# Optimization experiments

Hardware: AMD Instinct MI355X
Metric: run time of the kernel (lower is better)

Reference implementation:

```python
import jax, jax.numpy as jnp
import numpy as np

NM = 16  # n_modes


def setup_inputs() -> dict:
    key = jax.random.key(0)
    k1, k2, k3, k4 = jax.random.split(key, 4)
    B, M, N, I, O = 8, 256, 256, 64, 64
    std = 1.0 / (I * O)
    x = jax.random.normal(k1, (B, M, N, I), dtype=jnp.float32)
    w1 = jax.random.normal(k2, (I, O, NM, NM, 2), dtype=jnp.float32) * std
    w2 = jax.random.normal(k3, (I, O, NM, NM, 2), dtype=jnp.float32) * std
    lin_w = jax.random.normal(k4, (O, O), dtype=jnp.float32) * (1.0 / np.sqrt(O))
    lin_b = jnp.zeros((O,), dtype=jnp.float32)
    return {"x": x, "w1": w1, "w2": w2, "lin_w": lin_w, "lin_b": lin_b}


def _to_complex(w):
    return jax.lax.complex(w[..., 0], w[..., 1])


def reference(x, w1, w2, lin_w, lin_b):
    B, M, N, I = x.shape
    O = w1.shape[1]
    # [B, I, M, N]
    xt = jnp.transpose(x, (0, 3, 1, 2))
    # rfft over last two dims -> [B, I, M, N//2 + 1] complex
    x_ft = jnp.fft.rfft2(xt, s=(M, N), axes=(-2, -1))
    w1c = _to_complex(w1)  # [I, O, NM, NM]
    w2c = _to_complex(w2)
    # truncated complex matmuls over low modes (top rows) and high-negative modes (bottom rows)
    out_top = jnp.einsum('bixy,ioxy->boxy', x_ft[:, :, :NM, :NM], w1c)
    out_bot = jnp.einsum('bixy,ioxy->boxy', x_ft[:, :, -NM:, :NM], w2c)
    zeros_mid = jnp.zeros((B, O, M - 2 * NM, NM), dtype=out_top.dtype)
    rows = jnp.concatenate([out_top, zeros_mid, out_bot], axis=2)  # [B, O, M, NM]
    zeros_right = jnp.zeros((B, O, M, N // 2 + 1 - NM), dtype=out_top.dtype)
    out_ft = jnp.concatenate([rows, zeros_right], axis=3)  # [B, O, M, N//2+1]
    y = jnp.fft.irfft2(out_ft, s=(M, N), axes=(-2, -1))  # real [B, O, M, N]
    y = jnp.transpose(y, (0, 2, 3, 1))  # [B, M, N, O]
    res = y @ lin_w + lin_b
    return jax.nn.relu(y + res)
```

## Files before the change

### kernel.cpp

```cpp
#include <hip/hip_runtime.h>
#include <hip/hip_bf16.h>
#include <math.h>


#define TOFF  65536
#define XOFF  (TOFF + 4194304)
#define YOFF  (XOFF + 524288)
#define GOFF  (YOFF + 524288)

__global__ __launch_bounds__(256) void setup_tables(const float* __restrict__ lin_w,
                                                    float* __restrict__ ws) {
    int j = blockIdx.x * 256 + threadIdx.x;
    const float ANG = 0.024543692606170259f;
    if (j < 4096) {
        int n = j >> 4, ky = j & 15;
        int a = (n * ky) & 255;
        float s, c; sincosf(ANG * (float)a, &s, &c);
        int w = ky >> 2, jj = ky & 3;
        float* p = ws + w * 2048 + n * 8 + jj * 2;
        p[0] = c; p[1] = -s;
    } else if (j < 12288) {
        int e = j - 4096; int m = e >> 5, kx = e & 31;
        int kxe = kx + (kx < 16 ? 0 : 224);
        int a = (m * kxe) & 255;
        float s, c; sincosf(ANG * (float)a, &s, &c);
        int g = kx >> 2, kl = kx & 3;
        float* p = ws + 8192 + g * 2048 + m * 8 + kl * 2;
        p[0] = c; p[1] = -s;
    } else if (j < 20480) {
        int e = j - 12288; int kx = e >> 8, m = e & 255;
        int kxe = kx + (kx < 16 ? 0 : 224);
        int a = (kxe * m) & 255;
        float s, c; sincosf(ANG * (float)a, &s, &c);
        float* p = ws + 24576 + (kx * 256 + m) * 2;
        p[0] = c * (1.0f / 256.0f);
        p[1] = s * (1.0f / 256.0f);
    } else if (j < 28672) {
        int e = j - 20480; int f = e >> 8, n = e & 255;
        int ky = f >> 1, h = f & 1;
        int a = (ky * n) & 255;
        float s, c; sincosf(ANG * (float)a, &s, &c);
        float scale = (ky == 0 ? 1.0f : 2.0f) * (1.0f / 256.0f);
        ws[40960 + f * 256 + n] = h ? (-scale * s) : (scale * c);
    } else if (j < 32768) {
        int e = j - 28672;
        int op = e >> 6, o = e & 63;
        ws[49152 + e] = lin_w[e] + ((op == o) ? 1.0f : 0.0f);
    }
}

__global__ __launch_bounds__(256) void stageA(const float* __restrict__ x,
                                              const float* __restrict__ tabA,
                                              float* __restrict__ T) {
    __shared__ float xs[8192];
    int bid = blockIdx.x;
    int b = bid >> 8, m = bid & 255;
    int t = threadIdx.x;
    int i = t & 63, w = t >> 6;
    int lane = i;
    const float* twp = tabA + __builtin_amdgcn_readfirstlane(w * 2048);
    float aR[4], aI[4];
#pragma unroll
    for (int j = 0; j < 4; ++j) { aR[j] = 0.f; aI[j] = 0.f; }
    const float* xbase = x + (size_t)bid * 16384;
#pragma unroll
    for (int c = 0; c < 2; ++c) {
        if (c) __syncthreads();
        {
            const float* gsrc = xbase + c * 8192 + (w * 8) * 256 + lane * 4;
            float* ldst = xs + (w * 8) * 256;
#pragma unroll
            for (int q = 0; q < 8; ++q) {
                __builtin_amdgcn_global_load_lds(
                    (const __attribute__((address_space(1))) void*)(gsrc + q * 256),
                    (__attribute__((address_space(3))) void*)(uintptr_t)(ldst + q * 256),
                    16, 0, 0);
            }
        }
        asm volatile("s_waitcnt vmcnt(0)" ::: "memory");
        __syncthreads();
        const float* tc = twp + c * 1024;
#pragma unroll 4
        for (int nn = 0; nn < 128; ++nn) {
            float xv = xs[nn * 64 + i];
            const float* tp = tc + nn * 8;
            aR[0] = fmaf(tp[0], xv, aR[0]); aI[0] = fmaf(tp[1], xv, aI[0]);
            aR[1] = fmaf(tp[2], xv, aR[1]); aI[1] = fmaf(tp[3], xv, aI[1]);
            aR[2] = fmaf(tp[4], xv, aR[2]); aI[2] = fmaf(tp[5], xv, aI[2]);
            aR[3] = fmaf(tp[6], xv, aR[3]); aI[3] = fmaf(tp[7], xv, aI[3]);
        }
    }
    float2* Tb = (float2*)T;
#pragma unroll
    for (int j = 0; j < 4; ++j) {
        int ky = w * 4 + j;
        Tb[((size_t)(b * 16 + ky) * 256 + m) * 64 + i] = make_float2(aR[j], aI[j]);
    }
}

__global__ __launch_bounds__(512) void stageB(const float* __restrict__ T,
                                              const float* __restrict__ twF,
                                              float* __restrict__ X) {
    __shared__ float red[4 * 4 * 64 * 2];
    int bid = blockIdx.x;
    int b = bid >> 5;
    int ky = (bid >> 1) & 15;
    int half = bid & 1;
    int t = threadIdx.x, i = t & 63;
    int q = (t >> 6) & 3, h = t >> 8;
    int Q = half * 4 + q;
    const float2* Tp = (const float2*)T + (size_t)(b * 16 + ky) * 256 * 64 + i;
    const float* tw = twF + __builtin_amdgcn_readfirstlane(Q * 2048);
    float r0 = 0, r1 = 0, r2 = 0, r3 = 0;
    float s0 = 0, s1 = 0, s2 = 0, s3 = 0;
    int m0 = h * 128;
#pragma unroll 4
    for (int mm = 0; mm < 128; ++mm) {
        int m = m0 + mm;
        float2 tv = Tp[(size_t)m * 64];
        const float* tp = tw + m * 8;
        r0 = fmaf(tv.x, tp[0], fmaf(-tv.y, tp[1], r0));
        s0 = fmaf(tv.x, tp[1], fmaf( tv.y, tp[0], s0));
        r1 = fmaf(tv.x, tp[2], fmaf(-tv.y, tp[3], r1));
        s1 = fmaf(tv.x, tp[3], fmaf( tv.y, tp[2], s1));
        r2 = fmaf(tv.x, tp[4], fmaf(-tv.y, tp[5], r2));
        s2 = fmaf(tv.x, tp[5], fmaf( tv.y, tp[4], s2));
        r3 = fmaf(tv.x, tp[6], fmaf(-tv.y, tp[7], r3));
        s3 = fmaf(tv.x, tp[7], fmaf( tv.y, tp[6], s3));
    }
    float2* rp = (float2*)red + (q * 4) * 64 + i;
    if (h == 1) {
        rp[0 * 64] = make_float2(r0, s0);
        rp[1 * 64] = make_float2(r1, s1);
        rp[2 * 64] = make_float2(r2, s2);
        rp[3 * 64] = make_float2(r3, s3);
    }
    __syncthreads();
    if (h == 0) {
        float2 p0 = rp[0 * 64], p1 = rp[1 * 64], p2 = rp[2 * 64], p3 = rp[3 * 64];
        r0 += p0.x; s0 += p0.y; r1 += p1.x; s1 += p1.y;
        r2 += p2.x; s2 += p2.y; r3 += p3.x; s3 += p3.y;
        int kx0 = Q * 4;
        float2* Xb = (float2*)X;
        size_t base = ((size_t)(b * 16 + ky) * 32 + kx0) * 64 + i;
        Xb[base + 0 * 64] = make_float2(r0, s0);
        Xb[base + 1 * 64] = make_float2(r1, s1);
        Xb[base + 2 * 64] = make_float2(r2, s2);
        Xb[base + 3 * 64] = make_float2(r3, s3);
    }
}

__global__ __launch_bounds__(256) void stageC(const float* __restrict__ Xg,
                                              const float* __restrict__ w1,
                                              const float* __restrict__ w2,
                                              const float* __restrict__ Wf,
                                              float* __restrict__ Y2) {
    __shared__ float Ws[64 * 64 * 2];
    __shared__ float Xs[8 * 64 * 2];
    __shared__ float Ys[8 * 64 * 2];
    __shared__ float Wfs[64 * 64];
    int bid = blockIdx.x;
    int kx = bid & 31, ky = bid >> 5;
    int t = threadIdx.x;
    const float* wsrc = (kx < 16) ? w1 : w2;
    int xx = kx & 15;
#pragma unroll
    for (int q = 0; q < 16; ++q) {
        int p = t + q * 256;
        int ii = p >> 6, oo = p & 63;
        float2 wv = *(const float2*)(wsrc + ((size_t)(ii * 64 + oo) * 256 + xx * 16 + ky) * 2);
        ((float2*)Ws)[ii * 64 + oo] = wv;
    }
#pragma unroll
    for (int q = 0; q < 2; ++q) {
        int p = t + q * 256;
        int bb = p >> 6, ii = p & 63;
        ((float2*)Xs)[bb * 64 + ii] =
            ((const float2*)Xg)[((size_t)(bb * 16 + ky) * 32 + kx) * 64 + ii];
    }
#pragma unroll
    for (int q = 0; q < 16; ++q) Wfs[t + q * 256] = Wf[t + q * 256];
    __syncthreads();
    int o = t & 63, bg = t >> 6;
    float yr0 = 0, yi0 = 0, yr1 = 0, yi1 = 0;
    for (int ii = 0; ii < 64; ++ii) {
        float2 w = ((float2*)Ws)[ii * 64 + o];
        float2 xa = ((float2*)Xs)[bg * 64 + ii];
        float2 xb = ((float2*)Xs)[(bg + 4) * 64 + ii];
        yr0 = fmaf(xa.x, w.x, fmaf(-xa.y, w.y, yr0));
        yi0 = fmaf(xa.x, w.y, fmaf( xa.y, w.x, yi0));
        yr1 = fmaf(xb.x, w.x, fmaf(-xb.y, w.y, yr1));
        yi1 = fmaf(xb.x, w.y, fmaf( xb.y, w.x, yi1));
    }
    ((float2*)Ys)[bg * 64 + o] = make_float2(yr0, yi0);
    ((float2*)Ys)[(bg + 4) * 64 + o] = make_float2(yr1, yi1);
    __syncthreads();
    float zr0 = 0, zi0 = 0, zr1 = 0, zi1 = 0;
    for (int op = 0; op < 64; ++op) {
        float wf = Wfs[op * 64 + o];
        float2 ya = ((float2*)Ys)[bg * 64 + op];
        float2 yb = ((float2*)Ys)[(bg + 4) * 64 + op];
        zr0 = fmaf(ya.x, wf, zr0); zi0 = fmaf(ya.y, wf, zi0);
        zr1 = fmaf(yb.x, wf, zr1); zi1 = fmaf(yb.y, wf, zi1);
    }
    float2* Yb = (float2*)Y2;
    Yb[((size_t)(bg * 32 + kx) * 16 + ky) * 64 + o] = make_float2(zr0, zi0);
    Yb[((size_t)((bg + 4) * 32 + kx) * 16 + ky) * 64 + o] = make_float2(zr1, zi1);
}

__global__ __launch_bounds__(512) void stageD(const float* __restrict__ Y2,
                                              const float* __restrict__ twI,
                                              float* __restrict__ G) {
    __shared__ float Ysl[16 * 64 * 2];
    int bid = blockIdx.x;
    int b = bid >> 5, mg = bid & 31;
    int t = threadIdx.x, o = t & 63, ml = t >> 6;
    int m = mg * 8 + ml;
    float gr[16], gi[16];
#pragma unroll
    for (int k = 0; k < 16; ++k) { gr[k] = 0.f; gi[k] = 0.f; }
    for (int kx = 0; kx < 32; ++kx) {
        __syncthreads();
        const float2* src = (const float2*)Y2 + (size_t)(b * 32 + kx) * 1024;
#pragma unroll
        for (int qq = 0; qq < 2; ++qq) ((float2*)Ysl)[t + qq * 512] = src[t + qq * 512];
        __syncthreads();
        int off = __builtin_amdgcn_readfirstlane((kx * 256 + m) * 2);
        float c = twI[off], d = twI[off + 1];
#pragma unroll
        for (int ky = 0; ky < 16; ++ky) {
            float2 yv = ((float2*)Ysl)[ky * 64 + o];
            gr[ky] = fmaf(yv.x, c, fmaf(-yv.y, d, gr[ky]));
            gi[ky] = fmaf(yv.x, d, fmaf( yv.y, c, gi[ky]));
        }
    }
    float2* Gb = (float2*)G;
#pragma unroll
    for (int ky = 0; ky < 16; ++ky)
        Gb[((size_t)(b * 256 + m) * 16 + ky) * 64 + o] = make_float2(gr[ky], gi[ky]);
}

__global__ __launch_bounds__(256) void stageE(const float* __restrict__ G,
                                              const float* __restrict__ tabE,
                                              const float* __restrict__ lin_b,
                                              float* __restrict__ out) {
    __shared__ float Bs[32 * 256];
    __shared__ float Hs[32 * 64];
    int bid = blockIdx.x;
    int t = threadIdx.x;
    const float4* tE4 = (const float4*)tabE;
#pragma unroll
    for (int q = 0; q < 8; ++q) ((float4*)Bs)[t + q * 256] = tE4[t + q * 256];
    const float2* Gp = (const float2*)G + (size_t)bid * 1024;
#pragma unroll
    for (int q = 0; q < 4; ++q) {
        int p = t + q * 256;
        int ky = p >> 6, o = p & 63;
        float2 g = Gp[p];
        Hs[(2 * ky) * 64 + o] = g.x;
        Hs[(2 * ky + 1) * 64 + o] = g.y;
    }
    __syncthreads();
    int o4 = (t & 15) * 4, n0 = (t >> 4) * 16;
    float acc[16][4];
#pragma unroll
    for (int j = 0; j < 16; ++j) { acc[j][0] = acc[j][1] = acc[j][2] = acc[j][3] = 0.f; }
    for (int f = 0; f < 32; ++f) {
        float4 h = *(const float4*)(Hs + f * 64 + o4);
        const float* bp = Bs + f * 256 + n0;
        float4 a0 = *(const float4*)(bp);
        float4 a1 = *(const float4*)(bp + 4);
        float4 a2 = *(const float4*)(bp + 8);
        float4 a3 = *(const float4*)(bp + 12);
        float av[16] = {a0.x, a0.y, a0.z, a0.w, a1.x, a1.y, a1.z, a1.w,
                        a2.x, a2.y, a2.z, a2.w, a3.x, a3.y, a3.z, a3.w};
#pragma unroll
        for (int j = 0; j < 16; ++j) {
            acc[j][0] = fmaf(av[j], h.x, acc[j][0]);
            acc[j][1] = fmaf(av[j], h.y, acc[j][1]);
            acc[j][2] = fmaf(av[j], h.z, acc[j][2]);
            acc[j][3] = fmaf(av[j], h.w, acc[j][3]);
        }
    }
    float4 bias = *(const float4*)(lin_b + o4);
    float* outp = out + (size_t)bid * 256 * 64;
#pragma unroll
    for (int j = 0; j < 16; ++j) {
        int n = n0 + j;
        float4 r;
        r.x = fmaxf(acc[j][0] + bias.x, 0.f);
        r.y = fmaxf(acc[j][1] + bias.y, 0.f);
        r.z = fmaxf(acc[j][2] + bias.z, 0.f);
        r.w = fmaxf(acc[j][3] + bias.w, 0.f);
        *(float4*)(outp + (size_t)n * 64 + o4) = r;
    }
}

extern "C" void kernel_launch(void* const* d_in, const int* in_sizes, int n_in,
                              void* d_out, int out_size, void* d_ws, size_t ws_size,
                              hipStream_t stream) {
    const float* x     = (const float*)d_in[0];
    const float* w1    = (const float*)d_in[1];
    const float* w2    = (const float*)d_in[2];
    const float* lin_w = (const float*)d_in[3];
    const float* lin_b = (const float*)d_in[4];
    float* ws  = (float*)d_ws;
    float* out = (float*)d_out;

    float* T  = ws + TOFF;
    float* X  = ws + XOFF;
    float* Y2 = ws + YOFF;
    float* G  = ws + GOFF;

    setup_tables<<<128, 256, 0, stream>>>(lin_w, ws);
    stageA<<<2048, 256, 0, stream>>>(x, ws, T);
    stageB<<<256, 512, 0, stream>>>(T, ws + 8192, X);
    stageC<<<512, 256, 0, stream>>>(X, w1, w2, ws + 49152, Y2);
    stageD<<<256, 512, 0, stream>>>(Y2, ws + 24576, G);
    stageE<<<2048, 256, 0, stream>>>(G, ws + 40960, lin_b, out);
}
```

Baseline: 178.9 us.

## Split stageA over n-halves with direct global loads and LDS reduction

StageA no longer stages x rows in shared memory via global_load_lds. Each wave now reads x directly from global memory, handles one half of the n range, and accumulates 8 ky modes instead of 4. The two halves are summed through a small shared-memory reduction before writing T, and the twiddle table layout is changed to n*32+ky*2 to match. This removes the LDS staging and its barriers and halves the per-wave loop length. In exchange it doubles the accumulator registers and relies on the cache for the strided global loads.

New measurement: 162.3 us. 1.1x faster.

```diff
diff --git a/kernel.cpp b/kernel.cpp
--- a/kernel.cpp
+++ b/kernel.cpp
@@ -16,8 +16,7 @@
         int n = j >> 4, ky = j & 15;
         int a = (n * ky) & 255;
         float s, c; sincosf(ANG * (float)a, &s, &c);
-        int w = ky >> 2, jj = ky & 3;
-        float* p = ws + w * 2048 + n * 8 + jj * 2;
+        float* p = ws + n * 32 + ky * 2;
         p[0] = c; p[1] = -s;
     } else if (j < 12288) {
         int e = j - 4096; int m = e >> 5, kx = e & 31;
@@ -52,49 +51,42 @@
 __global__ __launch_bounds__(256) void stageA(const float* __restrict__ x,
                                               const float* __restrict__ tabA,
                                               float* __restrict__ T) {
-    __shared__ float xs[8192];
+    __shared__ float red[2 * 8 * 64 * 2];
     int bid = blockIdx.x;
     int b = bid >> 8, m = bid & 255;
     int t = threadIdx.x;
     int i = t & 63, w = t >> 6;
-    int lane = i;
-    const float* twp = tabA + __builtin_amdgcn_readfirstlane(w * 2048);
-    float aR[4], aI[4];
-#pragma unroll
-    for (int j = 0; j < 4; ++j) { aR[j] = 0.f; aI[j] = 0.f; }
-    const float* xbase = x + (size_t)bid * 16384;
-#pragma unroll
-    for (int c = 0; c < 2; ++c) {
-        if (c) __syncthreads();
-        {
-            const float* gsrc = xbase + c * 8192 + (w * 8) * 256 + lane * 4;
-            float* ldst = xs + (w * 8) * 256;
-#pragma unroll
-            for (int q = 0; q < 8; ++q) {
-                __builtin_amdgcn_global_load_lds(
-                    (const __attribute__((address_space(1))) void*)(gsrc + q * 256),
-                    (__attribute__((address_space(3))) void*)(uintptr_t)(ldst + q * 256),
-                    16, 0, 0);
-            }
+    int kh = w & 1, h = w >> 1;
+    const float* xp = x + (size_t)bid * 16384 + (size_t)h * 8192 + i;
+    const float* twp = tabA + __builtin_amdgcn_readfirstlane(h * 4096 + kh * 16);
+    float aR[8], aI[8];
+#pragma unroll
+    for (int j = 0; j < 8; ++j) { aR[j] = 0.f; aI[j] = 0.f; }
+#pragma unroll 4
+    for (int nn = 0; nn < 128; ++nn) {
+        float xv = xp[nn * 64];
+        const float* tp = twp + nn * 32;
+#pragma unroll
+        for (int j = 0; j < 8; ++j) {
+            aR[j] = fmaf(tp[2 * j], xv, aR[j]);
+            aI[j] = fmaf(tp[2 * j + 1], xv, aI[j]);
         }
-        asm volatile("s_waitcnt vmcnt(0)" ::: "memory");
-        __syncthreads();
-        const float* tc = twp + c * 1024;
-#pragma unroll 4
-        for (int nn = 0; nn < 128; ++nn) {
-            float xv = xs[nn * 64 + i];
-            const float* tp = tc + nn * 8;
-            aR[0] = fmaf(tp[0], xv, aR[0]); aI[0] = fmaf(tp[1], xv, aI[0]);
-            aR[1] = fmaf(tp[2], xv, aR[1]); aI[1] = fmaf(tp[3], xv, aI[1]);
-            aR[2] = fmaf(tp[4], xv, aR[2]); aI[2] = fmaf(tp[5], xv, aI[2]);
-            aR[3] = fmaf(tp[6], xv, aR[3]); aI[3] = fmaf(tp[7], xv, aI[3]);
+    }
+    float2* rp = (float2*)red + (kh * 8) * 64 + i;
+    if (h == 1) {
+#pragma unroll
+        for (int j = 0; j < 8; ++j) rp[j * 64] = make_float2(aR[j], aI[j]);
+    }
+    __syncthreads();
+    if (h == 0) {
+        float2* Tb = (float2*)T;
+#pragma unroll
+        for (int j = 0; j < 8; ++j) {
+            float2 p = rp[j * 64];
+            int ky = kh * 8 + j;
+            Tb[((size_t)(b * 16 + ky) * 256 + m) * 64 + i] =
+                make_float2(aR[j] + p.x, aI[j] + p.y);
         }
-    }
-    float2* Tb = (float2*)T;
-#pragma unroll
-    for (int j = 0; j < 4; ++j) {
-        int ky = w * 4 + j;
-        Tb[((size_t)(b * 16 + ky) * 256 + m) * 64 + i] = make_float2(aR[j], aI[j]);
     }
 }
 
```
